# Kernel tuning notes

Hardware: AMD Instinct MI355X
Metric: run time of the kernel (lower is better)

Reference implementation:

```python
import jax, jax.numpy as jnp
import numpy as np

DZ = 16
DX = 16
T = 256
K = 2 * T  # quad-form slots: slot 0 = prior, odd = integrated obs terms, even = transition terms
LOG2PI = float(np.log(2.0 * np.pi))


def setup_inputs() -> dict:
    key = jax.random.key(0)
    ks = jax.random.split(key, 20)

    def spd(k, d, s=0.5):
        L = jax.random.normal(k, (d, d))
        return s * (L @ L.T) / d + jnp.eye(d)

    sc = 1.0 / np.sqrt(DZ)
    return {
        "observations": jax.random.normal(ks[0], (T, DX)),
        "p_prior_mean": 0.1 * jax.random.normal(ks[1], (DZ,)),
        "p_prior_cov": spd(ks[2], DZ),
        "p_trans_w": 0.7 * sc * jax.random.normal(ks[3], (DZ, DZ)),
        "p_trans_b": 0.1 * jax.random.normal(ks[4], (DZ,)),
        "p_trans_cov": spd(ks[5], DZ),
        "p_em_w": sc * jax.random.normal(ks[6], (DX, DZ)),
        "p_em_b": 0.1 * jax.random.normal(ks[7], (DX,)),
        "p_em_cov": spd(ks[8], DX),
        "q_prior_mean": 0.1 * jax.random.normal(ks[9], (DZ,)),
        "q_prior_cov": spd(ks[10], DZ),
        "q_trans_w": 0.7 * sc * jax.random.normal(ks[11], (DZ, DZ)),
        "q_trans_b": 0.1 * jax.random.normal(ks[12], (DZ,)),
        "q_trans_cov": spd(ks[13], DZ),
        "q_em_w": sc * jax.random.normal(ks[14], (DX, DZ)),
        "q_em_b": 0.1 * jax.random.normal(ks[15], (DX,)),
        "q_em_cov": spd(ks[16], DX),
    }


def reference(observations, p_prior_mean, p_prior_cov, p_trans_w, p_trans_b, p_trans_cov,
              p_em_w, p_em_b, p_em_cov, q_prior_mean, q_prior_cov, q_trans_w, q_trans_b,
              q_trans_cov, q_em_w, q_em_b, q_em_cov):
    dz, dx = DZ, DX
    I = jnp.eye(dz, dtype=observations.dtype)

    def cterm(dim, det):  # -0.5*(d*log(2pi) + log det)
        return -0.5 * (dim * LOG2PI + jnp.log(det))

    p_tr_prec = jnp.linalg.inv(p_trans_cov)
    p_tr_det = jnp.linalg.det(p_trans_cov)
    p_em_prec = jnp.linalg.inv(p_em_cov)
    p_em_det = jnp.linalg.det(p_em_cov)
    q_tr_prec = jnp.linalg.inv(q_trans_cov)
    Om_obs = -0.5 * p_em_prec   # Omega of every observation term (linear-Gaussian emission)
    Om_tr = -0.5 * p_tr_prec    # Omega of every transition quad form

    def kupdate(m_pred, P_pred, y):  # Kalman measurement update under q
        S = q_em_w @ P_pred @ q_em_w.T + q_em_cov
        Kg = P_pred @ q_em_w.T @ jnp.linalg.inv(S)
        m = m_pred + Kg @ (y - q_em_w @ m_pred - q_em_b)
        P = (I - Kg @ q_em_w) @ P_pred
        return m, P

    # init: filtering + V
    m_f, P_f = kupdate(q_prior_mean, q_prior_cov, observations[0])
    const = cterm(dz, jnp.linalg.det(p_prior_cov)) + cterm(dx, p_em_det)
    As = jnp.zeros((K, dz, dz), observations.dtype).at[0].set(I)
    bs = jnp.zeros((K, dz), observations.dtype).at[0].set(-p_prior_mean)
    # static Omega stack (inactive slots have A=0,b=0 so they contribute exactly 0)
    odd = (jnp.arange(K) % 2 == 1)[:, None, None]
    Om = jnp.where(odd, Om_obs[None], Om_tr[None])
    Om = Om.at[0].set(-0.5 * jnp.linalg.inv(p_prior_cov))
    pend_b = p_em_b - observations[0]  # pending obs term: (Om_obs, p_em_w, pend_b)

    def step(carry, inp):
        As, bs, pend_b, m_f, P_f, const = carry
        y, t = inp
        # backward kernel from current filtering
        P_prec = jnp.linalg.inv(P_f)
        bprec = q_trans_w.T @ q_tr_prec @ q_trans_w + P_prec
        bcov = jnp.linalg.inv(bprec)
        cm = q_trans_w.T @ q_tr_prec
        B = bcov @ cm
        a = bcov @ (P_prec @ m_f - cm @ q_trans_b)
        # integrate all existing quad forms under backward: trace(Om A bcov A^T), A<-A@B, b<-A@a+b
        ACA = jnp.einsum('kij,jl,kml->kim', As, bcov, As)
        const = const + jnp.einsum('kij,kji->', Om, ACA)
        bs = jnp.einsum('kij,j->ki', As, a) + bs
        As = jnp.einsum('kij,jl->kil', As, B)
        # integrate pending observation term, append at slot 2t-1
        const = const + jnp.trace(Om_obs @ p_em_w @ bcov @ p_em_w.T)
        As = As.at[2 * t - 1].set(p_em_w @ B)
        bs = bs.at[2 * t - 1].set(p_em_w @ a + pend_b)
        # per-step constants
        const = (const + cterm(dx, p_em_det) + cterm(dz, p_tr_det)
                 - cterm(dz, jnp.linalg.det(bcov)) + 0.5 * dz
                 - 0.5 * jnp.trace(p_tr_prec @ p_trans_w @ bcov @ p_trans_w.T))
        # transition quad form at slot 2t
        As = As.at[2 * t].set(p_trans_w @ B - I)
        bs = bs.at[2 * t].set(p_trans_w @ a + p_trans_b)
        pend_b = p_em_b - y
        # Kalman filter step under q
        m_pred = q_trans_w @ m_f + q_trans_b
        P_pred = q_trans_w @ P_f @ q_trans_w.T + q_trans_cov
        m_f, P_f = kupdate(m_pred, P_pred, y)
        return (As, bs, pend_b, m_f, P_f, const), None

    ts = jnp.arange(1, T)
    (As, bs, pend_b, m_f, P_f, const), _ = jax.lax.scan(
        step, (As, bs, pend_b, m_f, P_f, const), (observations[1:], ts))

    const = const - cterm(dz, jnp.linalg.det(P_f))
    # expectation of quad forms under filtering (NOTE: trace(Om A P A), no final
    # transpose -- faithful to the source's _expect_quad_form_under_filtering)
    tr = jnp.einsum('kij,kjl,lm,kmi->', Om, As, P_f, As)
    u = jnp.einsum('kij,j->ki', As, m_f) + bs
    ev = jnp.einsum('ki,kij,kj->', u, Om, u)
    # pending observation term under filtering (same formula)
    up = p_em_w @ m_f + pend_b
    tr_p = jnp.trace(Om_obs @ p_em_w @ P_f @ p_em_w)
    ev_p = up @ Om_obs @ up
    return const + tr + ev + tr_p + ev_p + 0.5 * dz
```

## Files before the change

kernel.cpp:

```cpp
#include <hip/hip_runtime.h>
#include <cmath>

#define L2PI 1.8378770664093453f
#define CT16 (16.f * L2PI)

__device__ __align__(16) float g_Gstore[255 * 256];
__device__ float g_Pff[256], g_Om0[256], g_Omo[256], g_Omt[256], g_Ginf[256];
__device__ float g_partial, g_acc;
__device__ int g_tb;
__device__ unsigned g_cnt;

__device__ __forceinline__ float dAB(const float* A, const float* B, int i, int j) {
  float s = 0.f;
#pragma unroll
  for (int k = 0; k < 16; ++k) s = fmaf(A[i * 16 + k], B[k * 16 + j], s);
  return s;
}
__device__ __forceinline__ float dATB(const float* A, const float* B, int i, int j) {
  float s = 0.f;
#pragma unroll
  for (int k = 0; k < 16; ++k) s = fmaf(A[k * 16 + i], B[k * 16 + j], s);
  return s;
}
__device__ __forceinline__ float dABT(const float* A, const float* B, int i, int j) {
  float s = 0.f;
#pragma unroll
  for (int k = 0; k < 16; ++k) s = fmaf(A[i * 16 + k], B[j * 16 + k], s);
  return s;
}
__device__ __forceinline__ float mv(const float* M, const float* v, int r) {
  float s = 0.f;
#pragma unroll
  for (int k = 0; k < 16; ++k) s = fmaf(M[r * 16 + k], v[k], s);
  return s;
}
__device__ __forceinline__ float wave_sum(float v) {
#pragma unroll
  for (int off = 32; off; off >>= 1) v += __shfl_down(v, off);
  return v;
}
__device__ __forceinline__ float wave_max(float v) {
#pragma unroll
  for (int off = 32; off; off >>= 1) v = fmaxf(v, __shfl_down(v, off));
  return v;
}
__device__ __forceinline__ float rl(float v, int l) {
  return __int_as_float(__builtin_amdgcn_readlane(__float_as_int(v), l));
}

__device__ __forceinline__ float reg_gj_core(const float* __restrict__ src,
                                             float aI[4]) {
  const int wl = threadIdx.x & 63;
  const int col = wl & 15, rg = wl >> 4;
  float aA[4];
#pragma unroll
  for (int q = 0; q < 4; ++q) {
    const int r = rg + 4 * q;
    aA[q] = src[r * 16 + col];
    aI[q] = (r == col) ? 1.f : 0.f;
  }
  float det = 1.f;
#pragma unroll
  for (int k = 0; k < 16; ++k) {
    const int kq = k >> 2, kr = k & 3;
    const float piv = rl(aA[kq], (kr << 4) | k);
    det *= piv;
    const float rp = 1.f / piv;
    const float pA = __shfl(aA[kq], (kr << 4) | col);
    const float pI = __shfl(aI[kq], (kr << 4) | col);
    float f[4];
    f[0] = __shfl(aA[0], (rg << 4) | k);
    f[1] = __shfl(aA[1], (rg << 4) | k);
    f[2] = __shfl(aA[2], (rg << 4) | k);
    f[3] = __shfl(aA[3], (rg << 4) | k);
#pragma unroll
    for (int q = 0; q < 4; ++q) {
      const float tq = f[q] * rp;
      const float nA = fmaf(-tq, pA, aA[q]);
      const float nI = fmaf(-tq, pI, aI[q]);
      if (q == kq) {
        const bool isp = (rg == kr);
        aA[q] = isp ? pA * rp : nA;
        aI[q] = isp ? pI * rp : nI;
      } else {
        aA[q] = nA;
        aI[q] = nI;
      }
    }
  }
  return det;
}

__device__ __forceinline__ float reg_gj_inv(const float* __restrict__ src,
                                            float* __restrict__ dst) {
  const int wl = threadIdx.x & 63;
  const int col = wl & 15, rg = wl >> 4;
  float aI[4];
  const float det = reg_gj_core(src, aI);
#pragma unroll
  for (int q = 0; q < 4; ++q) dst[(rg + 4 * q) * 16 + col] = aI[q];
  return det;
}

template <int MODE>
__device__ __forceinline__ float gj_inv_mul(const float* __restrict__ src,
                                            const float* __restrict__ Bm,
                                            float* __restrict__ dst,
                                            float* __restrict__ dstT) {
  const int wl = threadIdx.x & 63;
  const int col = wl & 15, rg = wl >> 4;
  float aI[4];
  const float det = reg_gj_core(src, aI);
  float part[16];
#pragma unroll
  for (int ii = 0; ii < 16; ++ii) {
    float s = 0.f;
#pragma unroll
    for (int q = 0; q < 4; ++q) {
      const int k = rg + 4 * q;
      s = fmaf(MODE == 0 ? Bm[k * 16 + ii] : Bm[ii * 16 + k], aI[q], s);
    }
    part[ii] = s;
  }
#pragma unroll
  for (int ii = 0; ii < 16; ++ii) {
    part[ii] += __shfl_xor(part[ii], 16);
    part[ii] += __shfl_xor(part[ii], 32);
  }
  if (rg == 0) {
    dst[0 * 16 + col] = part[0];  dst[1 * 16 + col] = part[1];
    dst[2 * 16 + col] = part[2];  dst[3 * 16 + col] = part[3];
    if (dstT) {
      float4* p4 = (float4*)(dstT + col * 16);
      p4[0] = make_float4(part[0], part[1], part[2], part[3]);
      p4[1] = make_float4(part[4], part[5], part[6], part[7]);
      p4[2] = make_float4(part[8], part[9], part[10], part[11]);
      p4[3] = make_float4(part[12], part[13], part[14], part[15]);
    }
  } else if (rg == 1) {
    dst[4 * 16 + col] = part[4];  dst[5 * 16 + col] = part[5];
    dst[6 * 16 + col] = part[6];  dst[7 * 16 + col] = part[7];
  } else if (rg == 2) {
    dst[8 * 16 + col] = part[8];  dst[9 * 16 + col] = part[9];
    dst[10 * 16 + col] = part[10]; dst[11 * 16 + col] = part[11];
  } else {
    dst[12 * 16 + col] = part[12]; dst[13 * 16 + col] = part[13];
    dst[14 * 16 + col] = part[14]; dst[15 * 16 + col] = part[15];
  }
  return det;
}

__global__ void __launch_bounds__(256)
lgq_fwd(const float* __restrict__ obs,
        const float* __restrict__ ppm, const float* __restrict__ ppc,
        const float* __restrict__ ptw, const float* __restrict__ ptb,
        const float* __restrict__ ptc, const float* __restrict__ pew,
        const float* __restrict__ peb, const float* __restrict__ pec,
        const float* __restrict__ qpm, const float* __restrict__ qpc,
        const float* __restrict__ qtw, const float* __restrict__ qtb,
        const float* __restrict__ qtc, const float* __restrict__ qew,
        const float* __restrict__ qeb, const float* __restrict__ qec) {
  const int e = threadIdx.x;
  const int i = e >> 4, j = e & 15;
  const int wid = e >> 6;
  const int lane = e & 63;

  __shared__ float W[256], WT[256], Qm[256], Hm[256], Rm[256], Em[256], EmT[256],
      PwmT[256];
  __shared__ float HW[256], QHt[256], HQH[256], TmpB[256], TmpBT[256];
  __shared__ float Om0[256], Omo[256], Omt[256], Fo[256], Ft[256], Nm[256],
      NmT[256], EOm[256];
  __shared__ float Sm[256], Pf[256];
  __shared__ float WP[256], WPT[256], U[256], Ppred[256], Smat[256], PHt[256];
  __shared__ float Pi[256], Si[256], Gm[256], GmT[256], Kgm[256], Mm[256];
  __shared__ float T1m[256], T1mT[256], NGm[256], NGmT[256];
  __shared__ float sObs[256 * 16];
  __shared__ float detPArr[256], detSArr[256], d3all[256];
  __shared__ float uB1[252 * 16], pB1[252 * 16], pC1[252 * 16];
  __shared__ float mfs1[252 * 16], rvs1[252 * 16];
  __shared__ float mf[16], mfN[16], rv[16], pb[16], bqv[16], bemv[16], pbemv[16],
      ptbv[16];
  __shared__ float w2[16], q2[16], mpred[16], av[16], hv[16];
  __shared__ float EOpb[16], resid[16], tv1[16], tv2[16], Opf[16];
  __shared__ float ca[16], mca[16], nca[16], c1[16], cg1[16], qc[16], epbm[16];
  __shared__ float red[4], red2[4], red3[4], dets[6];
  __shared__ float sc_const, sc_c, ctb, sh_cstep;
  __shared__ float ld_pprior, ld_ptr, ld_pem, ld_Q, ld_R, ld_qprior, ld_Pf;
  __shared__ float sh_detS, sh_tstep_inf;
  __shared__ int sh_frozen;

  W[e] = qtw[e]; Qm[e] = qtc[e]; Hm[e] = qew[e]; Rm[e] = qec[e];
  Em[e] = pew[e];
  WT[e] = qtw[j * 16 + i]; EmT[e] = pew[j * 16 + i]; PwmT[e] = ptw[j * 16 + i];
  {
    const float4* o4 = (const float4*)obs;
    float4* s4 = (float4*)sObs;
#pragma unroll
    for (int q = 0; q < 4; ++q) s4[e + 256 * q] = o4[e + 256 * q];
  }
  if (e < 16) { bqv[e] = qtb[e]; bemv[e] = qeb[e]; pbemv[e] = peb[e]; ptbv[e] = ptb[e]; }
  if (e == 0) { sh_frozen = 0; g_acc = 0.f; g_cnt = 0u; }
  __syncthreads();
  HW[e] = dABT(Hm, WT, i, j);
  TmpB[e] = dABT(Hm, Qm, i, j);
  __syncthreads();
  HQH[e] = dABT(TmpB, Hm, i, j) + Rm[e];
  QHt[e] = TmpB[j * 16 + i];
  __syncthreads();
  if (wid == 0) {
    float d0 = reg_gj_inv(ppc, Pi);
    float d1 = reg_gj_inv(ptc, Si);
    if (e == 0) { dets[0] = d0; dets[1] = d1; }
  } else if (wid == 1) {
    float d2 = reg_gj_inv(pec, Gm);
    float d3 = reg_gj_inv(qtc, Kgm);
    if (e == 64) { dets[2] = d2; dets[3] = d3; }
  } else if (wid == 2) {
    float d4 = reg_gj_inv(qec, T1m);
    float d5 = reg_gj_inv(qpc, NGm);
    if (e == 128) { dets[4] = d4; dets[5] = d5; }
  }
  __syncthreads();
  Om0[e] = -0.5f * Pi[e];
  Omt[e] = -0.5f * Si[e];
  Omo[e] = -0.5f * Gm[e];
  g_Om0[e] = Om0[e]; g_Omo[e] = Omo[e]; g_Omt[e] = Omt[e];
  Sm[e] = Om0[e];
  {
    const float v = -0.5f * dABT(Gm, EmT, i, j);
    TmpB[e] = v; TmpBT[j * 16 + i] = v;
  }
  {
    const float v = -0.5f * dABT(Si, PwmT, i, j);
    Nm[e] = v; NmT[j * 16 + i] = v;
  }
  EOm[e] = -0.5f * dABT(EmT, Gm, i, j);
  if (e == 0) {
    ld_pprior = logf(dets[0]); ld_ptr = logf(dets[1]); ld_pem = logf(dets[2]);
    ld_Q = logf(dets[3]); ld_R = logf(dets[4]); ld_qprior = logf(dets[5]);
  }
  __syncthreads();
  Fo[e] = dABT(EmT, TmpBT, i, j);
  Ft[e] = dABT(PwmT, NmT, i, j);
  if (e < 16) w2[e] = mv(NmT, ptbv, e);
  else if (e < 32) q2[e - 16] = mv(Omt, ptbv, e - 16);
  else if (e < 48) rv[e - 32] = -mv(Om0, ppm, e - 32);
  else if (e < 64) pb[e - 48] = pbemv[e - 48] - sObs[e - 48];
  {
    const int rr = e & 15, tg = e >> 4;
#pragma unroll
    for (int it = 0; it < 16; ++it) {
      const int tt = it * 16 + tg;
      float s = 0.f;
#pragma unroll
      for (int k = 0; k < 16; ++k)
        s = fmaf(Omo[rr * 16 + k], pbemv[k] - sObs[tt * 16 + k], s);
      s *= (pbemv[rr] - sObs[tt * 16 + rr]);
      s += __shfl_xor(s, 1); s += __shfl_xor(s, 2);
      s += __shfl_xor(s, 4); s += __shfl_xor(s, 8);
      if (rr == 0) d3all[tt] = s;
    }
  }
  __syncthreads();
  if (e == 0) {
    float s = 0.f, ct = 0.f;
    for (int k = 0; k < 16; ++k) { s = fmaf(ppm[k], rv[k], s); ct = fmaf(ptbv[k], q2[k], ct); }
    sc_c = -s;
    ctb = ct;
    sc_const = -0.5f * (CT16 + ld_pprior) - 0.5f * (CT16 + ld_pem);
    sh_cstep = 8.f - 0.5f * CT16 - 0.5f * (ld_pem + ld_ptr);
  }
  if (e < 16) mpred[e] = qpm[e];
  {
    const float v = dABT(Hm, qpc, i, j);
    TmpB[e] = v; TmpBT[j * 16 + i] = v;
  }
  __syncthreads();
  Smat[e] = dABT(TmpB, Hm, i, j) + Rm[e];
  if (e < 16) resid[e] = sObs[e] - bemv[e] - mv(Hm, mpred, e);
  __syncthreads();
  if (wid == 0) {
    float d = gj_inv_mul<0>(Smat, TmpB, Kgm, nullptr);
    if (e == 0) sh_detS = d;
  }
  __syncthreads();
  Pf[e] = qpc[e] - dABT(Kgm, TmpBT, i, j);
  if (e < 16) { mf[e] = mpred[e] + mv(Kgm, resid, e); mfN[e] = mf[e]; }
  if (e == 0) ld_Pf = ld_qprior + ld_R - logf(sh_detS);
  __syncthreads();

  float d1acc = 0.f, tacc = 0.f, fd2 = 0.f, facc = 0.f;
  int t = 1;
  for (; t < 256; ++t) {
    const float* y = sObs + t * 16;
    WP[e] = dABT(W, Pf, i, j);
    WPT[e] = dABT(Pf, W, i, j);
    U[e] = dABT(HW, Pf, i, j);
    if (t > 1) {
      const float sN = dABT(GmT, T1mT, i, j) - NGmT[e] - NGm[e] + Omt[e];
      const float sd = fabsf(sN - Sm[e]);
      Sm[e] = sN;
      const float vm = wave_max(sd);
      if (lane == 0) red3[wid] = vm;
      d1acc = fmaf(Mm[e] * av[i], av[j], d1acc);
      if (e < 16) {
        float s = -q2[e];
#pragma unroll
        for (int k = 0; k < 16; ++k) {
          s = fmaf(T1mT[e * 16 + k], av[k], s);
          s = fmaf(GmT[e * 16 + k], hv[k], s);
          s = fmaf(-Nm[e * 16 + k], av[k], s);
        }
        rv[e] = s;
      } else if (e < 32) {
        fd2 = fmaf(av[e - 16], hv[e - 16], fd2);
        mf[e - 16] = mfN[e - 16];
      } else if (e < 48) {
        mpred[e - 32] = bqv[e - 32] + mv(W, mfN, e - 32);
      }
    } else {
      if (e < 16) mpred[e] = bqv[e] + mv(W, mf, e);
    }
    __syncthreads();
    Ppred[e] = dABT(WP, W, i, j) + Qm[e];
    Smat[e] = dABT(U, HW, i, j) + HQH[e];
    PHt[e] = dABT(WP, HW, i, j) + QHt[e];
    if (e < 16) resid[e] = y[e] - bemv[e] - mv(Hm, mpred, e);
    if (e == 0 && t >= 4) {
      const float pfd = fmaxf(fmaxf(red2[0], red2[1]), fmaxf(red2[2], red2[3]));
      const float sdm = fmaxf(fmaxf(red3[0], red3[1]), fmaxf(red3[2], red3[3]));
      if (pfd < 3e-3f && sdm < 3e-2f) sh_frozen = 1;
    }
    __syncthreads();
    if (sh_frozen) break;
    if (wid == 0) {
      const float d = gj_inv_mul<1>(Ppred, WPT, Gm, GmT);
      if (e == 0) detPArr[t] = d;
    } else if (wid == 1) {
      const float d = gj_inv_mul<1>(Smat, PHt, Kgm, nullptr);
      if (e == 64) detSArr[t] = d;
    } else if (wid == 2) {
      const int wl = e & 63;
#pragma unroll
      for (int q = 0; q < 4; ++q) { const int x = wl + 64 * q; Mm[x] = Sm[x] + Fo[x] + Ft[x]; }
      if (wl < 16) EOpb[wl] = mv(EOm, pb, wl);
    }
    __syncthreads();
    {
      const float bc = Pf[e] - dABT(Gm, WPT, i, j);
      tacc = fmaf(Mm[e], bc, tacc);
      const float pfN = Ppred[e] - dABT(Kgm, PHt, i, j);
      const float df = fabsf(pfN - Pf[e]);
      Pf[e] = pfN;
      const float vm = wave_max(df);
      if (lane == 0) red2[wid] = vm;
    }
    {
      const float v1 = dABT(Mm, GmT, i, j);
      T1m[e] = v1; T1mT[j * 16 + i] = v1;
      const float v2 = dABT(Nm, GmT, i, j);
      NGm[e] = v2; NGmT[j * 16 + i] = v2;
    }
    g_Gstore[(t - 1) * 256 + e] = Gm[e];
    if (e < 16) av[e] = mf[e] - mv(Gm, mpred, e);
    else if (e < 32) mfN[e - 16] = mpred[e - 16] + mv(Kgm, resid, e - 16);
    else if (e < 48) hv[e - 32] = rv[e - 32] + EOpb[e - 32] + w2[e - 32];
    else if (e < 64) pb[e - 48] = pbemv[e - 48] - y[e - 48];
    __syncthreads();
  }

  const int tb = t;
  if (sh_frozen) {
    const int NT = 256 - tb;
    const int AA = NT & ~3;
    const int r16 = e & 15, kslot = e >> 4;
    T1m[e] = dAB(Kgm, Hm, i, j);
    NGm[e] = ((i == j) ? 1.f : 0.f) - dABT(Gm, WT, i, j);
    Mm[e] = Sm[e] + Fo[e] + Ft[e];
    if (e < 16) ca[e] = -mv(Gm, bqv, e);
    else if (e < 32) epbm[e - 16] = mv(EOm, pbemv, e - 16);
    __syncthreads();
    Smat[e] = W[e] - dABT(T1m, WT, i, j);
    Pi[e] = dAB(Mm, NGm, i, j);
    Si[e] = dAB(Nm, NGm, i, j);
    {
      const float bcf = Pf[e] - dABT(Gm, WPT, i, j);
      const float v = wave_sum(Mm[e] * bcf);
      if (lane == 0) red[wid] = v;
    }
    if (e < 16) mca[e] = mv(Mm, ca, e);
    else if (e < 32) nca[e - 16] = mv(Nm, ca, e - 16);
    else if (e < 48) {
      const int r = e - 32;
      c1[r] = bqv[r] - mv(T1m, bqv, r) - mv(Kgm, bemv, r);
    }
    __syncthreads();
    U[e] = dATB(Gm, Pi, i, j) - Si[e];
    Ppred[e] = dATB(Gm, EOm, i, j);
    Fo[e] = dAB(Smat, Smat, i, j);
    HW[e] = dAB(Gm, Gm, i, j);
    if (e < 16) {
      float s = 0.f;
#pragma unroll
      for (int k = 0; k < 16; ++k)
        s = fmaf(GmT[e * 16 + k], w2[k] + mca[k] + epbm[k], s);
      cg1[e] = s - nca[e] - q2[e];
    } else if (e < 32) {
      const int r = e - 16;
      qc[r] = mca[r] + 2.f * w2[r] + 2.f * epbm[r];
    } else if (e < 48) {
      mfs1[e - 32] = mf[e - 32];
    } else if (e < 64) {
      rvs1[e - 48] = rv[e - 48];
    }
    if (e == 0) sh_tstep_inf = red[0] + red[1] + red[2] + red[3];
    {
      float kgrow[16];
#pragma unroll
      for (int k2 = 0; k2 < 16; ++k2) kgrow[k2] = Kgm[r16 * 16 + k2];
      const float c1r = c1[r16];
      for (int k = 1 + kslot; k <= NT; k += 16) {
        const float* yc = sObs + (tb - 1 + k) * 16;
        float s = c1r;
#pragma unroll
        for (int k2 = 0; k2 < 16; ++k2) s = fmaf(kgrow[k2], yc[k2], s);
        uB1[k * 16 + r16] = s;
      }
    }
    __syncthreads();
    Ft[e] = dAB(Fo, Fo, i, j);
    QHt[e] = dAB(HW, HW, i, j);
    {
      float a1row[16];
#pragma unroll
      for (int k2 = 0; k2 < 16; ++k2) a1row[k2] = Smat[r16 * 16 + k2];
      for (int k = 2 + kslot; k <= NT; k += 16) {
        const float* up = uB1 + (k - 1) * 16;
        float s = uB1[k * 16 + r16];
#pragma unroll
        for (int k2 = 0; k2 < 16; ++k2) s = fmaf(a1row[k2], up[k2], s);
        pB1[k * 16 + r16] = s;
      }
    }
    __syncthreads();
    {
      float a2row[16];
#pragma unroll
      for (int k2 = 0; k2 < 16; ++k2) a2row[k2] = Fo[r16 * 16 + k2];
      for (int k = 4 + kslot; k <= NT; k += 16) {
        const float* pp = pB1 + (k - 2) * 16;
        float s = pB1[k * 16 + r16];
#pragma unroll
        for (int k2 = 0; k2 < 16; ++k2) s = fmaf(a2row[k2], pp[k2], s);
        pC1[k * 16 + r16] = s;
      }
    }
    __syncthreads();
    if (wid == 0 && AA >= 4) {
      const int r = lane & 15;
      float a4row[16];
#pragma unroll
      for (int k2 = 0; k2 < 16; ++k2) a4row[k2] = Ft[r * 16 + k2];
      float x = mf[r];
      float d0 = pC1[4 * 16 + r];
      float d1 = (AA >= 8) ? pC1[8 * 16 + r] : 0.f;
      for (int k = 4; k <= AA; k += 4) {
        const float d2 = (k + 8 <= AA) ? pC1[(k + 8) * 16 + r] : 0.f;
        float s0 = d0, s1 = 0.f, s2 = 0.f, s3 = 0.f;
#pragma unroll
        for (int k2 = 0; k2 < 16; k2 += 4) {
          s0 = fmaf(a4row[k2],     rl(x, k2),     s0);
          s1 = fmaf(a4row[k2 + 1], rl(x, k2 + 1), s1);
          s2 = fmaf(a4row[k2 + 2], rl(x, k2 + 2), s2);
          s3 = fmaf(a4row[k2 + 3], rl(x, k2 + 3), s3);
        }
        x = (s0 + s1) + (s2 + s3);
        if (lane < 16) mfs1[k * 16 + r] = x;
        d0 = d1; d1 = d2;
      }
    }
    __syncthreads();
    {
      float a1row[16], a2row[16];
#pragma unroll
      for (int k2 = 0; k2 < 16; ++k2) {
        a1row[k2] = Smat[r16 * 16 + k2];
        a2row[k2] = Fo[r16 * 16 + k2];
      }
      for (int a = 4 * kslot; a <= NT; a += 64) {
        const float* mfp = mfs1 + a * 16;
        if (a + 1 <= NT) {
          float s = uB1[(a + 1) * 16 + r16];
#pragma unroll
          for (int k2 = 0; k2 < 16; ++k2) s = fmaf(a1row[k2], mfp[k2], s);
          mfs1[(a + 1) * 16 + r16] = s;
        }
        if (a + 2 <= NT) {
          float s = pB1[(a + 2) * 16 + r16];
#pragma unroll
          for (int k2 = 0; k2 < 16; ++k2) s = fmaf(a2row[k2], mfp[k2], s);
          mfs1[(a + 2) * 16 + r16] = s;
        }
      }
    }
    __syncthreads();
    {
      float a2row[16];
#pragma unroll
      for (int k2 = 0; k2 < 16; ++k2) a2row[k2] = Fo[r16 * 16 + k2];
      for (int a = 4 * kslot; a <= NT; a += 64) {
        if (a + 3 <= NT) {
          const float* mfp = mfs1 + (a + 1) * 16;
          float s = pB1[(a + 3) * 16 + r16];
#pragma unroll
          for (int k2 = 0; k2 < 16; ++k2) s = fmaf(a2row[k2], mfp[k2], s);
          mfs1[(a + 3) * 16 + r16] = s;
        }
      }
    }
    __syncthreads();
    {
      float b1row[16], georow[16];
#pragma unroll
      for (int k2 = 0; k2 < 16; ++k2) {
        b1row[k2] = U[r16 * 16 + k2];
        georow[k2] = Ppred[r16 * 16 + k2];
      }
      const float cg1r = cg1[r16];
      for (int k = 1 + kslot; k <= NT; k += 16) {
        const float* mfp = mfs1 + (k - 1) * 16;
        const float* yp = sObs + (tb - 2 + k) * 16;
        float s = cg1r;
#pragma unroll
        for (int k2 = 0; k2 < 16; ++k2) {
          s = fmaf(b1row[k2], mfp[k2], s);
          s = fmaf(-georow[k2], yp[k2], s);
        }
        uB1[k * 16 + r16] = s;
      }
    }
    if (e < 16) { mf[e] = mfs1[NT * 16 + e]; pb[e] = pbemv[e] - sObs[255 * 16 + e]; }
    __syncthreads();
    {
      float gtrow[16];
#pragma unroll
      for (int k2 = 0; k2 < 16; ++k2) gtrow[k2] = GmT[r16 * 16 + k2];
      for (int k = 2 + kslot; k <= NT; k += 16) {
        const float* wp = uB1 + (k - 1) * 16;
        float s = uB1[k * 16 + r16];
#pragma unroll
        for (int k2 = 0; k2 < 16; ++k2) s = fmaf(gtrow[k2], wp[k2], s);
        pB1[k * 16 + r16] = s;
      }
    }
    __syncthreads();
    {
      float gt2row[16];
#pragma unroll
      for (int k2 = 0; k2 < 16; ++k2) gt2row[k2] = HW[k2 * 16 + r16];
      for (int k = 4 + kslot; k <= NT; k += 16) {
        const float* wp = pB1 + (k - 2) * 16;
        float s = pB1[k * 16 + r16];
#pragma unroll
        for (int k2 = 0; k2 < 16; ++k2) s = fmaf(gt2row[k2], wp[k2], s);
        pC1[k * 16 + r16] = s;
      }
    }
    __syncthreads();
    if (wid == 0 && AA >= 4) {
      const int r = lane & 15;
      float g4row[16];
#pragma unroll
      for (int k2 = 0; k2 < 16; ++k2) g4row[k2] = QHt[k2 * 16 + r];
      float x = rv[r];
      float d0 = pC1[4 * 16 + r];
      float d1 = (AA >= 8) ? pC1[8 * 16 + r] : 0.f;
      for (int k = 4; k <= AA; k += 4) {
        const float d2 = (k + 8 <= AA) ? pC1[(k + 8) * 16 + r] : 0.f;
        float s0 = d0, s1 = 0.f, s2 = 0.f, s3 = 0.f;
#pragma unroll
        for (int k2 = 0; k2 < 16; k2 += 4) {
          s0 = fmaf(g4row[k2],     rl(x, k2),     s0);
          s1 = fmaf(g4row[k2 + 1], rl(x, k2 + 1), s1);
          s2 = fmaf(g4row[k2 + 2], rl(x, k2 + 2), s2);
          s3 = fmaf(g4row[k2 + 3], rl(x, k2 + 3), s3);
        }
        x = (s0 + s1) + (s2 + s3);
        if (lane < 16) rvs1[k * 16 + r] = x;
        d0 = d1; d1 = d2;
      }
    }
    __syncthreads();
    {
      float gtrow[16], gt2row[16];
#pragma unroll
      for (int k2 = 0; k2 < 16; ++k2) {
        gtrow[k2] = GmT[r16 * 16 + k2];
        gt2row[k2] = HW[k2 * 16 + r16];
      }
      for (int a = 4 * kslot; a <= NT; a += 64) {
        const float* rp = rvs1 + a * 16;
        if (a + 1 <= NT) {
          float s = uB1[(a + 1) * 16 + r16];
#pragma unroll
          for (int k2 = 0; k2 < 16; ++k2) s = fmaf(gtrow[k2], rp[k2], s);
          rvs1[(a + 1) * 16 + r16] = s;
        }
        if (a + 2 <= NT) {
          float s = pB1[(a + 2) * 16 + r16];
#pragma unroll
          for (int k2 = 0; k2 < 16; ++k2) s = fmaf(gt2row[k2], rp[k2], s);
          rvs1[(a + 2) * 16 + r16] = s;
        }
      }
    }
    __syncthreads();
    {
      float gt2row[16];
#pragma unroll
      for (int k2 = 0; k2 < 16; ++k2) gt2row[k2] = HW[k2 * 16 + r16];
      for (int a = 4 * kslot; a <= NT; a += 64) {
        if (a + 3 <= NT) {
          const float* rp = rvs1 + (a + 1) * 16;
          float s = pB1[(a + 3) * 16 + r16];
#pragma unroll
          for (int k2 = 0; k2 < 16; ++k2) s = fmaf(gt2row[k2], rp[k2], s);
          rvs1[(a + 3) * 16 + r16] = s;
        }
      }
    }
    __syncthreads();
    {
      float avrow[16], mavrow[16], eorow[16];
#pragma unroll
      for (int k2 = 0; k2 < 16; ++k2) {
        avrow[k2] = NGm[r16 * 16 + k2];
        mavrow[k2] = Pi[r16 * 16 + k2];
        eorow[k2] = EOm[r16 * 16 + k2];
      }
      const float car = ca[r16], qcr = qc[r16];
      for (int k = 1 + kslot; k <= NT; k += 16) {
        const float* mfp = mfs1 + (k - 1) * 16;
        const float* yp = sObs + (tb - 2 + k) * 16;
        float avr = car, qr = qcr + 2.f * rvs1[(k - 1) * 16 + r16];
#pragma unroll
        for (int k2 = 0; k2 < 16; ++k2) {
          avr = fmaf(avrow[k2], mfp[k2], avr);
          qr = fmaf(mavrow[k2], mfp[k2], qr);
          qr = fmaf(-2.f * eorow[k2], yp[k2], qr);
        }
        facc = fmaf(avr, qr, facc);
      }
    }
    if (e < 16) rv[e] = rvs1[NT * 16 + e];
    __syncthreads();
  } else {
    const float sN = dABT(GmT, T1mT, i, j) - NGmT[e] - NGm[e] + Omt[e];
    Sm[e] = sN;
    d1acc = fmaf(Mm[e] * av[i], av[j], d1acc);
    if (e < 16) {
      float s = -q2[e];
#pragma unroll
      for (int k = 0; k < 16; ++k) {
        s = fmaf(T1mT[e * 16 + k], av[k], s);
        s = fmaf(GmT[e * 16 + k], hv[k], s);
        s = fmaf(-Nm[e * 16 + k], av[k], s);
      }
      rv[e] = s;
    } else if (e < 32) {
      fd2 = fmaf(av[e - 16], hv[e - 16], fd2);
      mf[e - 16] = mfN[e - 16];
    }
    __syncthreads();
  }

  const int n = tb - 1;
  if (e >= 1 && e <= n) {
    detPArr[e] = logf(detPArr[e]);
    detSArr[e] = logf(detSArr[e]);
  }
  {
    const float vA = d1acc + 2.f * fd2 + facc;
    const float vB = tacc;
    const float vC = (e < 255) ? d3all[e] : 0.f;
    const float sA = wave_sum(vA);
    const float sB = wave_sum(vB);
    const float sC = wave_sum(vC);
    if (lane == 0) { red[wid] = sA; red2[wid] = sB; red3[wid] = sC; }
  }
  __syncthreads();
  if (e == 0) {
    const float dsum = red[0] + red[1] + red[2] + red[3];
    const float tsum = red2[0] + red2[1] + red2[2] + red2[3];
    const float d3tot = red3[0] + red3[1] + red3[2] + red3[3];
    float lpf = ld_Pf;
    float sum_ldb = 0.f, ldbl = 0.f;
    for (int s2 = 1; s2 <= n; ++s2) {
      ldbl = lpf + ld_Q - detPArr[s2];
      sum_ldb += ldbl;
      lpf = detPArr[s2] + ld_R - detSArr[s2];
    }
    float sc = sc_const + tsum + (float)n * sh_cstep + 0.5f * sum_ldb;
    if (tb < 256) sc += (float)(256 - tb) * (sh_tstep_inf + sh_cstep + 0.5f * ldbl);
    sc_const = sc;
    ld_Pf = lpf;
    sc_c += dsum + d3tot + 255.f * ctb;
  }
  __syncthreads();

  g_Pff[e] = Pf[e];
  g_Ginf[e] = Gm[e];
  if (e == 0) g_tb = tb;
  WP[e] = dABT(Pf, EmT, i, j);
  if (e < 16) tv1[e] = mv(Sm, mf, e);
  else if (e < 32) tv2[e - 16] = pb[e - 16] + mv(Em, mf, e - 16);
  __syncthreads();
  {
    const float v = wave_sum(EOm[e] * WP[e]);
    if (lane == 0) red[wid] = v;
  }
  if (e < 16) Opf[e] = mv(Omo, tv2, e);
  __syncthreads();
  if (e == 0) {
    const float tr_p = red[0] + red[1] + red[2] + red[3];
    float ev1 = 0.f, ev2 = 0.f, evp = 0.f;
    for (int k = 0; k < 16; ++k) {
      ev1 = fmaf(mf[k], tv1[k], ev1);
      ev2 = fmaf(rv[k], mf[k], ev2);
      evp = fmaf(tv2[k], Opf[k], evp);
    }
    g_partial = sc_const + 0.5f * (CT16 + ld_Pf) + (ev1 + 2.f * ev2 + sc_c)
                + tr_p + evp + 8.f;
  }
}

__global__ void __launch_bounds__(256)
lgq_trace(const float* __restrict__ pew, const float* __restrict__ ptw,
          float* __restrict__ out) {
  const int e = threadIdx.x, i = e >> 4, j = e & 15, b = blockIdx.x;
  const int lane = e & 63, wid = e >> 6;
  __shared__ float Pfs[256], OmA[256], OmtS[256], EmS[256], PwS[256], GinfS[256];
  __shared__ float Xb[2][256], Bb[2][256];
  __shared__ float Sm1[256], Sf[256], A1[256], A2[256];
  __shared__ float T1v[256], NGv[256], Kxv[256], S2v[256];
  __shared__ float redt[4];
  int tb = g_tb;
  tb = (tb < 1) ? 1 : (tb > 256 ? 256 : tb);
  Pfs[e] = g_Pff[e];
  OmtS[e] = g_Omt[e];
  EmS[e] = pew[e];
  PwS[e] = ptw[e];
  GinfS[e] = g_Ginf[e];
  OmA[e] = (b == 0) ? g_Om0[e] : g_Omo[e];
  Xb[0][e] = (i == j) ? 1.f : 0.f;
  Bb[0][e] = g_Ginf[e];
  __syncthreads();
  int E = (b >= tb) ? (255 - b) : (256 - tb);
  int xc = 0, bc2 = 0;
  while (E) {
    Xb[xc ^ 1][e] = (E & 1) ? dAB(Xb[xc], Bb[bc2], i, j) : Xb[xc][e];
    if (E > 1) Bb[bc2 ^ 1][e] = dAB(Bb[bc2], Bb[bc2], i, j);
    __syncthreads();
    xc ^= 1; bc2 ^= 1;
    E >>= 1;
  }
  if (b >= tb) {
    Sf[e] = Xb[xc][e];
    Sm1[e] = dAB(GinfS, Xb[xc], i, j);
    __syncthreads();
  } else {
    int cur = xc;
    for (int s2 = tb - 1; s2 >= b + 1; --s2) {
      const float4* gr = (const float4*)(g_Gstore + (s2 - 1) * 256 + i * 16);
      const float4 a0 = gr[0], a1 = gr[1], a2 = gr[2], a3 = gr[3];
      const float* Xc = Xb[cur];
      float s = 0.f;
      s = fmaf(a0.x, Xc[0 * 16 + j], s);  s = fmaf(a0.y, Xc[1 * 16 + j], s);
      s = fmaf(a0.z, Xc[2 * 16 + j], s);  s = fmaf(a0.w, Xc[3 * 16 + j], s);
      s = fmaf(a1.x, Xc[4 * 16 + j], s);  s = fmaf(a1.y, Xc[5 * 16 + j], s);
      s = fmaf(a1.z, Xc[6 * 16 + j], s);  s = fmaf(a1.w, Xc[7 * 16 + j], s);
      s = fmaf(a2.x, Xc[8 * 16 + j], s);  s = fmaf(a2.y, Xc[9 * 16 + j], s);
      s = fmaf(a2.z, Xc[10 * 16 + j], s); s = fmaf(a2.w, Xc[11 * 16 + j], s);
      s = fmaf(a3.x, Xc[12 * 16 + j], s); s = fmaf(a3.y, Xc[13 * 16 + j], s);
      s = fmaf(a3.z, Xc[14 * 16 + j], s); s = fmaf(a3.w, Xc[15 * 16 + j], s);
      Xb[cur ^ 1][e] = s;
      __syncthreads();
      cur ^= 1;
    }
    Sf[e] = Xb[cur][e];
    if (b >= 1) {
      const float4* gr = (const float4*)(g_Gstore + (b - 1) * 256 + i * 16);
      const float4 a0 = gr[0], a1 = gr[1], a2 = gr[2], a3 = gr[3];
      const float* Xc = Xb[cur];
      float s = 0.f;
      s = fmaf(a0.x, Xc[0 * 16 + j], s);  s = fmaf(a0.y, Xc[1 * 16 + j], s);
      s = fmaf(a0.z, Xc[2 * 16 + j], s);  s = fmaf(a0.w, Xc[3 * 16 + j], s);
      s = fmaf(a1.x, Xc[4 * 16 + j], s);  s = fmaf(a1.y, Xc[5 * 16 + j], s);
      s = fmaf(a1.z, Xc[6 * 16 + j], s);  s = fmaf(a1.w, Xc[7 * 16 + j], s);
      s = fmaf(a2.x, Xc[8 * 16 + j], s);  s = fmaf(a2.y, Xc[9 * 16 + j], s);
      s = fmaf(a2.z, Xc[10 * 16 + j], s); s = fmaf(a2.w, Xc[11 * 16 + j], s);
      s = fmaf(a3.x, Xc[12 * 16 + j], s); s = fmaf(a3.y, Xc[13 * 16 + j], s);
      s = fmaf(a3.z, Xc[14 * 16 + j], s); s = fmaf(a3.w, Xc[15 * 16 + j], s);
      Sm1[e] = s;
    } else {
      Sm1[e] = Xb[cur][e];
    }
    __syncthreads();
  }
  if (b == 0) {
    A1[e] = Sm1[e];
    A2[e] = 0.f;
  } else {
    A1[e] = dAB(EmS, Sm1, i, j);
    A2[e] = dAB(PwS, Sm1, i, j) - Sf[e];
  }
  __syncthreads();
  T1v[e] = dAB(OmA, A1, i, j);
  NGv[e] = dAB(Pfs, A1, i, j);
  Kxv[e] = dAB(OmtS, A2, i, j);
  S2v[e] = dAB(Pfs, A2, i, j);
  __syncthreads();
  float val = T1v[e] * NGv[j * 16 + i] + Kxv[e] * S2v[j * 16 + i];
  val = wave_sum(val);
  if (lane == 0) redt[wid] = val;
  __syncthreads();
  if (e == 0) {
    atomicAdd(&g_acc, redt[0] + redt[1] + redt[2] + redt[3]);
    __threadfence();
    const unsigned o = atomicAdd(&g_cnt, 1u);
    if (o == 255u) {
      const float acc = atomicAdd(&g_acc, 0.f);
      out[0] = g_partial + acc;
    }
  }
}

extern "C" void kernel_launch(void* const* d_in, const int* in_sizes, int n_in,
                              void* d_out, int out_size, void* d_ws, size_t ws_size,
                              hipStream_t stream) {
  (void)in_sizes; (void)n_in; (void)out_size; (void)d_ws; (void)ws_size;
  lgq_fwd<<<dim3(1), dim3(256), 0, stream>>>(
      (const float*)d_in[0], (const float*)d_in[1], (const float*)d_in[2],
      (const float*)d_in[3], (const float*)d_in[4], (const float*)d_in[5],
      (const float*)d_in[6], (const float*)d_in[7], (const float*)d_in[8],
      (const float*)d_in[9], (const float*)d_in[10], (const float*)d_in[11],
      (const float*)d_in[12], (const float*)d_in[13], (const float*)d_in[14],
      (const float*)d_in[15], (const float*)d_in[16]);
  lgq_trace<<<dim3(256), dim3(256), 0, stream>>>((const float*)d_in[6],
                                                 (const float*)d_in[3],
                                                 (float*)d_out);
}
```

Measured before the change: 98.73 us.

## Cut barriers by merging setup matmuls and fusing dependent recurrence passes

The fourth wave now computes HW and HQH's intermediate while the other waves do Gauss-Jordan inversions, and redundant temporaries are replaced by existing matrices (EOm, WP/WPT). In the batched tail, dependent passes are fused by precomputing composed matrices (Fo·Smat, HW·Gm, Gm^T·U, Gm^T·Ppred) so two-step recurrences become one pass. The final trace reduction is folded into the existing reduction. The aim is to remove several __syncthreads and serial passes, at the cost of extra small matmuls and more register rows per thread.

New measurement: 98.53 us. Within noise of the previous version (-0.2%).

```diff
diff --git a/kernel.cpp b/kernel.cpp
--- a/kernel.cpp
+++ b/kernel.cpp
@@ -167,7 +167,7 @@
 
   __shared__ float W[256], WT[256], Qm[256], Hm[256], Rm[256], Em[256], EmT[256],
       PwmT[256];
-  __shared__ float HW[256], QHt[256], HQH[256], TmpB[256], TmpBT[256];
+  __shared__ float HW[256], QHt[256], HQH[256], TmpB[256];
   __shared__ float Om0[256], Omo[256], Omt[256], Fo[256], Ft[256], Nm[256],
       NmT[256], EOm[256];
   __shared__ float Sm[256], Pf[256];
@@ -176,8 +176,8 @@
   __shared__ float T1m[256], T1mT[256], NGm[256], NGmT[256];
   __shared__ float sObs[256 * 16];
   __shared__ float detPArr[256], detSArr[256], d3all[256];
-  __shared__ float uB1[252 * 16], pB1[252 * 16], pC1[252 * 16];
-  __shared__ float mfs1[252 * 16], rvs1[252 * 16];
+  __shared__ float uB1[253 * 16], pB1[253 * 16], pC1[253 * 16];
+  __shared__ float mfs1[253 * 16], rvs1[253 * 16];
   __shared__ float mf[16], mfN[16], rv[16], pb[16], bqv[16], bemv[16], pbemv[16],
       ptbv[16];
   __shared__ float w2[16], q2[16], mpred[16], av[16], hv[16];
@@ -200,12 +200,6 @@
   }
   if (e < 16) { bqv[e] = qtb[e]; bemv[e] = qeb[e]; pbemv[e] = peb[e]; ptbv[e] = ptb[e]; }
   if (e == 0) { sh_frozen = 0; g_acc = 0.f; g_cnt = 0u; }
-  __syncthreads();
-  HW[e] = dABT(Hm, WT, i, j);
-  TmpB[e] = dABT(Hm, Qm, i, j);
-  __syncthreads();
-  HQH[e] = dABT(TmpB, Hm, i, j) + Rm[e];
-  QHt[e] = TmpB[j * 16 + i];
   __syncthreads();
   if (wid == 0) {
     float d0 = reg_gj_inv(ppc, Pi);
@@ -219,18 +213,25 @@
     float d4 = reg_gj_inv(qec, T1m);
     float d5 = reg_gj_inv(qpc, NGm);
     if (e == 128) { dets[4] = d4; dets[5] = d5; }
-  }
-  __syncthreads();
+  } else {
+    const int l = e - 192;
+#pragma unroll
+    for (int q = 0; q < 4; ++q) {
+      const int idx = l + 64 * q;
+      const int ii = idx >> 4, jj = idx & 15;
+      HW[idx] = dABT(Hm, WT, ii, jj);
+      TmpB[idx] = dABT(Hm, Qm, ii, jj);
+    }
+  }
+  __syncthreads();
+  HQH[e] = dABT(TmpB, Hm, i, j) + Rm[e];
+  QHt[e] = TmpB[j * 16 + i];
   Om0[e] = -0.5f * Pi[e];
   Omt[e] = -0.5f * Si[e];
   Omo[e] = -0.5f * Gm[e];
   g_Om0[e] = Om0[e]; g_Omo[e] = Omo[e]; g_Omt[e] = Omt[e];
   Sm[e] = Om0[e];
   {
-    const float v = -0.5f * dABT(Gm, EmT, i, j);
-    TmpB[e] = v; TmpBT[j * 16 + i] = v;
-  }
-  {
     const float v = -0.5f * dABT(Si, PwmT, i, j);
     Nm[e] = v; NmT[j * 16 + i] = v;
   }
@@ -240,12 +241,15 @@
     ld_Q = logf(dets[3]); ld_R = logf(dets[4]); ld_qprior = logf(dets[5]);
   }
   __syncthreads();
-  Fo[e] = dABT(EmT, TmpBT, i, j);
+  Fo[e] = dABT(EmT, EOm, i, j);
   Ft[e] = dABT(PwmT, NmT, i, j);
+  WP[e] = dABT(Hm, qpc, i, j);
+  WPT[e] = dABT(qpc, Hm, i, j);
   if (e < 16) w2[e] = mv(NmT, ptbv, e);
   else if (e < 32) q2[e - 16] = mv(Omt, ptbv, e - 16);
   else if (e < 48) rv[e - 32] = -mv(Om0, ppm, e - 32);
   else if (e < 64) pb[e - 48] = pbemv[e - 48] - sObs[e - 48];
+  else if (e < 80) mpred[e - 64] = qpm[e - 64];
   {
     const int rr = e & 15, tg = e >> 4;
 #pragma unroll
@@ -270,21 +274,18 @@
     sc_const = -0.5f * (CT16 + ld_pprior) - 0.5f * (CT16 + ld_pem);
     sh_cstep = 8.f - 0.5f * CT16 - 0.5f * (ld_pem + ld_ptr);
   }
-  if (e < 16) mpred[e] = qpm[e];
-  {
-    const float v = dABT(Hm, qpc, i, j);
-    TmpB[e] = v; TmpBT[j * 16 + i] = v;
-  }
-  __syncthreads();
-  Smat[e] = dABT(TmpB, Hm, i, j) + Rm[e];
-  if (e < 16) resid[e] = sObs[e] - bemv[e] - mv(Hm, mpred, e);
+  Smat[e] = dABT(WP, Hm, i, j) + Rm[e];
+  if (e >= 16 && e < 32) {
+    const int r = e - 16;
+    resid[r] = sObs[r] - bemv[r] - mv(Hm, mpred, r);
+  }
   __syncthreads();
   if (wid == 0) {
-    float d = gj_inv_mul<0>(Smat, TmpB, Kgm, nullptr);
+    float d = gj_inv_mul<0>(Smat, WP, Kgm, nullptr);
     if (e == 0) sh_detS = d;
   }
   __syncthreads();
-  Pf[e] = qpc[e] - dABT(Kgm, TmpBT, i, j);
+  Pf[e] = qpc[e] - dABT(Kgm, WPT, i, j);
   if (e < 16) { mf[e] = mpred[e] + mv(Kgm, resid, e); mfN[e] = mf[e]; }
   if (e == 0) ld_Pf = ld_qprior + ld_R - logf(sh_detS);
   __syncthreads();
@@ -430,6 +431,9 @@
     __syncthreads();
     Ft[e] = dAB(Fo, Fo, i, j);
     QHt[e] = dAB(HW, HW, i, j);
+    T1m[e] = dATB(Gm, U, i, j);
+    T1mT[e] = dATB(Gm, Ppred, i, j);
+    if (e < 16) tv1[e] = mv(GmT, cg1, e);
     {
       float a1row[16];
 #pragma unroll
@@ -443,6 +447,8 @@
       }
     }
     __syncthreads();
+    NGmT[e] = dAB(Fo, Smat, i, j);
+    WPT[e] = dAB(HW, Gm, i, j);
     {
       float a2row[16];
 #pragma unroll
@@ -481,11 +487,12 @@
     }
     __syncthreads();
     {
-      float a1row[16], a2row[16];
+      float a1row[16], a2row[16], a3row[16];
 #pragma unroll
       for (int k2 = 0; k2 < 16; ++k2) {
         a1row[k2] = Smat[r16 * 16 + k2];
         a2row[k2] = Fo[r16 * 16 + k2];
+        a3row[k2] = NGmT[r16 * 16 + k2];
       }
       for (int a = 4 * kslot; a <= NT; a += 64) {
         const float* mfp = mfs1 + a * 16;
@@ -501,58 +508,53 @@
           for (int k2 = 0; k2 < 16; ++k2) s = fmaf(a2row[k2], mfp[k2], s);
           mfs1[(a + 2) * 16 + r16] = s;
         }
-      }
-    }
-    __syncthreads();
-    {
-      float a2row[16];
-#pragma unroll
-      for (int k2 = 0; k2 < 16; ++k2) a2row[k2] = Fo[r16 * 16 + k2];
-      for (int a = 4 * kslot; a <= NT; a += 64) {
         if (a + 3 <= NT) {
-          const float* mfp = mfs1 + (a + 1) * 16;
+          const float* up = uB1 + (a + 1) * 16;
           float s = pB1[(a + 3) * 16 + r16];
 #pragma unroll
-          for (int k2 = 0; k2 < 16; ++k2) s = fmaf(a2row[k2], mfp[k2], s);
+          for (int k2 = 0; k2 < 16; ++k2) {
+            s = fmaf(a3row[k2], mfp[k2], s);
+            s = fmaf(a2row[k2], up[k2], s);
+          }
           mfs1[(a + 3) * 16 + r16] = s;
         }
       }
     }
     __syncthreads();
     {
-      float b1row[16], georow[16];
+      float b1row[16], georow[16], gtbrow[16], gtgrow[16];
 #pragma unroll
       for (int k2 = 0; k2 < 16; ++k2) {
         b1row[k2] = U[r16 * 16 + k2];
         georow[k2] = Ppred[r16 * 16 + k2];
-      }
-      const float cg1r = cg1[r16];
+        gtbrow[k2] = T1m[r16 * 16 + k2];
+        gtgrow[k2] = T1mT[r16 * 16 + k2];
+      }
+      const float cg1r = cg1[r16], cgtr = tv1[r16];
       for (int k = 1 + kslot; k <= NT; k += 16) {
         const float* mfp = mfs1 + (k - 1) * 16;
         const float* yp = sObs + (tb - 2 + k) * 16;
-        float s = cg1r;
+        float w = cg1r;
 #pragma unroll
         for (int k2 = 0; k2 < 16; ++k2) {
-          s = fmaf(b1row[k2], mfp[k2], s);
-          s = fmaf(-georow[k2], yp[k2], s);
-        }
-        uB1[k * 16 + r16] = s;
+          w = fmaf(b1row[k2], mfp[k2], w);
+          w = fmaf(-georow[k2], yp[k2], w);
+        }
+        uB1[k * 16 + r16] = w;
+        if (k >= 2) {
+          const float* mfp2 = mfp - 16;
+          const float* yp2 = yp - 16;
+          float w2v = w + cgtr;
+#pragma unroll
+          for (int k2 = 0; k2 < 16; ++k2) {
+            w2v = fmaf(gtbrow[k2], mfp2[k2], w2v);
+            w2v = fmaf(-gtgrow[k2], yp2[k2], w2v);
+          }
+          pB1[k * 16 + r16] = w2v;
+        }
       }
     }
     if (e < 16) { mf[e] = mfs1[NT * 16 + e]; pb[e] = pbemv[e] - sObs[255 * 16 + e]; }
-    __syncthreads();
-    {
-      float gtrow[16];
-#pragma unroll
-      for (int k2 = 0; k2 < 16; ++k2) gtrow[k2] = GmT[r16 * 16 + k2];
-      for (int k = 2 + kslot; k <= NT; k += 16) {
-        const float* wp = uB1 + (k - 1) * 16;
-        float s = uB1[k * 16 + r16];
-#pragma unroll
-        for (int k2 = 0; k2 < 16; ++k2) s = fmaf(gtrow[k2], wp[k2], s);
-        pB1[k * 16 + r16] = s;
-      }
-    }
     __syncthreads();
     {
       float gt2row[16];
@@ -592,11 +594,12 @@
     }
     __syncthreads();
     {
-      float gtrow[16], gt2row[16];
+      float gtrow[16], gt2row[16], gt3row[16];
 #pragma unroll
       for (int k2 = 0; k2 < 16; ++k2) {
         gtrow[k2] = GmT[r16 * 16 + k2];
         gt2row[k2] = HW[k2 * 16 + r16];
+        gt3row[k2] = WPT[k2 * 16 + r16];
       }
       for (int a = 4 * kslot; a <= NT; a += 64) {
         const float* rp = rvs1 + a * 16;
@@ -612,24 +615,20 @@
           for (int k2 = 0; k2 < 16; ++k2) s = fmaf(gt2row[k2], rp[k2], s);
           rvs1[(a + 2) * 16 + r16] = s;
         }
-      }
-    }
-    __syncthreads();
-    {
-      float gt2row[16];
-#pragma unroll
-      for (int k2 = 0; k2 < 16; ++k2) gt2row[k2] = HW[k2 * 16 + r16];
-      for (int a = 4 * kslot; a <= NT; a += 64) {
         if (a + 3 <= NT) {
-          const float* rp = rvs1 + (a + 1) * 16;
+          const float* up = uB1 + (a + 1) * 16;
           float s = pB1[(a + 3) * 16 + r16];
 #pragma unroll
-          for (int k2 = 0; k2 < 16; ++k2) s = fmaf(gt2row[k2], rp[k2], s);
+          for (int k2 = 0; k2 < 16; ++k2) {
+            s = fmaf(gt3row[k2], rp[k2], s);
+            s = fmaf(gt2row[k2], up[k2], s);
+          }
           rvs1[(a + 3) * 16 + r16] = s;
         }
       }
     }
     __syncthreads();
+    WP[e] = dABT(Pf, EmT, i, j);
     {
       float avrow[16], mavrow[16], eorow[16];
 #pragma unroll
@@ -658,6 +657,7 @@
     const float sN = dABT(GmT, T1mT, i, j) - NGmT[e] - NGm[e] + Omt[e];
     Sm[e] = sN;
     d1acc = fmaf(Mm[e] * av[i], av[j], d1acc);
+    WP[e] = dABT(Pf, EmT, i, j);
     if (e < 16) {
       float s = -q2[e];
 #pragma unroll
@@ -679,14 +679,21 @@
     detPArr[e] = logf(detPArr[e]);
     detSArr[e] = logf(detSArr[e]);
   }
+  g_Pff[e] = Pf[e];
+  g_Ginf[e] = Gm[e];
+  if (e == 0) g_tb = tb;
+  if (e < 16) tv1[e] = mv(Sm, mf, e);
+  else if (e < 32) tv2[e - 16] = pb[e - 16] + mv(Em, mf, e - 16);
   {
     const float vA = d1acc + 2.f * fd2 + facc;
     const float vB = tacc;
     const float vC = (e < 255) ? d3all[e] : 0.f;
+    const float vD = EOm[e] * WP[e];
     const float sA = wave_sum(vA);
     const float sB = wave_sum(vB);
     const float sC = wave_sum(vC);
-    if (lane == 0) { red[wid] = sA; red2[wid] = sB; red3[wid] = sC; }
+    const float sD = wave_sum(vD);
+    if (lane == 0) { red[wid] = sA; red2[wid] = sB; red3[wid] = sC; dets[wid] = sD; }
   }
   __syncthreads();
   if (e == 0) {
@@ -705,24 +712,12 @@
     sc_const = sc;
     ld_Pf = lpf;
     sc_c += dsum + d3tot + 255.f * ctb;
-  }
-  __syncthreads();
-
-  g_Pff[e] = Pf[e];
-  g_Ginf[e] = Gm[e];
-  if (e == 0) g_tb = tb;
-  WP[e] = dABT(Pf, EmT, i, j);
-  if (e < 16) tv1[e] = mv(Sm, mf, e);
-  else if (e < 32) tv2[e - 16] = pb[e - 16] + mv(Em, mf, e - 16);
-  __syncthreads();
-  {
-    const float v = wave_sum(EOm[e] * WP[e]);
-    if (lane == 0) red[wid] = v;
-  }
-  if (e < 16) Opf[e] = mv(Omo, tv2, e);
+  } else if (e >= 16 && e < 32) {
+    Opf[e - 16] = mv(Omo, tv2, e - 16);
+  }
   __syncthreads();
   if (e == 0) {
-    const float tr_p = red[0] + red[1] + red[2] + red[3];
+    const float tr_p = dets[0] + dets[1] + dets[2] + dets[3];
     float ev1 = 0.f, ev2 = 0.f, evp = 0.f;
     for (int k = 0; k < 16; ++k) {
       ev1 = fmaf(mf[k], tv1[k], ev1);
```
